# Kernel optimization log

Measured on AMD Instinct MI355X. Metric: run time of the kernel, lower is better.

Reference implementation:

```python
import jax, jax.numpy as jnp
import numpy as np

B, Q, V, T = 96, 96, 197, 77   # image batch, text batch, visual tokens, text tokens
DV, DT, E = 768, 768, 512      # visual_size, textual_size, embed_size


def l2norm(x):
    # F.normalize(t, dim=-1, p=2) with eps=1e-12
    n = jnp.linalg.norm(x, axis=-1, keepdims=True)
    return x / jnp.maximum(n, 1e-12)


def setup_inputs() -> dict:
    key = jax.random.key(0)
    ks = jax.random.split(key, 12)
    sv = 1.0 / np.sqrt(DV).astype(np.float32)
    st = 1.0 / np.sqrt(DT).astype(np.float32)
    return {
        "visual_cls": jax.random.normal(ks[0], (B, DV), jnp.float32),
        "visual_tokens": jax.random.normal(ks[1], (B, V, DV), jnp.float32),
        "textual_cls": jax.random.normal(ks[2], (Q, DT), jnp.float32),
        "textual_tokens": jax.random.normal(ks[3], (Q, T, DT), jnp.float32),
        "Wv_cls": jax.random.normal(ks[4], (E, DV), jnp.float32) * sv,
        "bv_cls": jnp.zeros((E,), jnp.float32),
        "Wt_cls": jax.random.normal(ks[5], (E, DT), jnp.float32) * st,
        "bt_cls": jnp.zeros((E,), jnp.float32),
        "Wv_tok": jax.random.normal(ks[6], (E, DV), jnp.float32) * sv,
        "bv_tok": jnp.zeros((E,), jnp.float32),
        "Wt_tok": jax.random.normal(ks[7], (E, DT), jnp.float32) * st,
        "bt_tok": jnp.zeros((E,), jnp.float32),
        "text_length": jax.random.randint(ks[8], (Q,), 5, T + 1, jnp.int32),
    }


def reference(visual_cls, visual_tokens, textual_cls, textual_tokens,
              Wv_cls, bv_cls, Wt_cls, bt_cls,
              Wv_tok, bv_tok, Wt_tok, bt_tok, text_length):
    # Linear projections (torch nn.Linear: y = x @ W.T + b)
    v_cls = visual_cls @ Wv_cls.T + bv_cls            # [b, e]
    t_cls = textual_cls @ Wt_cls.T + bt_cls           # [q, e]
    v_tok = l2norm(jnp.einsum('bvd,ed->bve', visual_tokens, Wv_tok) + bv_tok)   # [b, v, e]
    t_tok = l2norm(jnp.einsum('qtd,ed->qte', textual_tokens, Wt_tok) + bt_tok)  # [q, t, e]

    # valid-token mask from caption lengths: mask[q, t]
    mask = (jnp.arange(T)[None, :] < text_length[:, None]).astype(v_tok.dtype)

    # fine-grained token similarity: [b, q, v, t], masked on text tokens
    logits = jnp.einsum('bve,qte->bqvt', v_tok, t_tok) * mask[None, :, None, :]

    text_sum = mask.sum(-1)                           # [q]
    t2v = logits.max(axis=2).sum(axis=2) / text_sum[None, :]   # [b, q]
    v2t = logits.max(axis=3).sum(axis=2) / V                   # [b, q]
    return (v_cls, t_cls, t2v, v2t)
```

## Files before the change

kernel.cpp:

```cpp
#include <hip/hip_runtime.h>

#define NB 96
#define NQ 96
#define NV 197
#define NT 77
#define DK 768
#define DE 512

typedef __attribute__((ext_vector_type(8))) short s16x8;
typedef __attribute__((ext_vector_type(4))) float f32x4;

__device__ __forceinline__ unsigned short f2bf(float f) {
  union { float f; unsigned int u; } v; v.f = f;
  unsigned int u = v.u;
  unsigned int r = u + 0x7fffu + ((u >> 16) & 1u);
  return (unsigned short)(r >> 16);
}

__device__ __forceinline__ unsigned int pack2bf(float a, float b) {
  return (unsigned int)f2bf(a) | ((unsigned int)f2bf(b) << 16);
}

#define GL16(gp, lp, off)                                                \
  __builtin_amdgcn_global_load_lds(                                      \
      (const __attribute__((address_space(1))) void*)(gp),               \
      (__attribute__((address_space(3))) void*)(lp), 16, (off), 0)

__global__ __launch_bounds__(256) void cvt_bf16_kernel(
    const float* __restrict__ src, unsigned short* __restrict__ dst, int n4) {
  int i = blockIdx.x * 256 + threadIdx.x;
  if (i < n4) {
    float4 x = ((const float4*)src)[i];
    ushort4 h;
    h.x = f2bf(x.x); h.y = f2bf(x.y); h.z = f2bf(x.z); h.w = f2bf(x.w);
    ((ushort4*)dst)[i] = h;
  }
}

__global__ __launch_bounds__(256) void cls_kernel(
    const float* __restrict__ X, const float* __restrict__ W,
    const float* __restrict__ bias, float* __restrict__ out) {
  __shared__ float xs[DK];
  const int row = blockIdx.x;
  const float* xr = X + (long)row * DK;
  for (int i = threadIdx.x; i < DK; i += 256) xs[i] = xr[i];
  __syncthreads();
  for (int c = threadIdx.x; c < DE; c += 256) {
    const float* wr = W + (long)c * DK;
    float s = 0.f;
    #pragma unroll 4
    for (int k = 0; k < DK; k += 4) {
      float4 w4 = *(const float4*)(wr + k);
      s += xs[k] * w4.x + xs[k + 1] * w4.y + xs[k + 2] * w4.z + xs[k + 3] * w4.w;
    }
    out[(long)row * DE + c] = s + bias[c];
  }
}

__global__ __launch_bounds__(256, 2) void proj_norm_kernel(
    const float* __restrict__ X, const unsigned short* __restrict__ Wb,
    const float* __restrict__ bias, unsigned short* __restrict__ Y, int M) {
  __shared__ __align__(16) unsigned short Ws[512 * 64];
  __shared__ __align__(16) unsigned short Xs[64 * 64];
  __shared__ float ssq_lds[4][64];

  const int tid = threadIdx.x;
  const int wave = tid >> 6;
  const int lane = tid & 63;
  const int l15 = lane & 15;
  const int quad = lane >> 4;
  const long row0 = (long)blockIdx.x * 64;

  const int sub = lane >> 3;
  const int swz = ((lane & 7) ^ sub) << 3;
  const unsigned short* pw_base = Wb + (long)(wave * 8 + sub) * DK + swz;

  const int xrow_a = tid >> 3;
  const int xrow_b = xrow_a + 32;
  const int xs8 = tid & 7;
  long gra = row0 + xrow_a; if (gra > M - 1) gra = M - 1;
  long grb = row0 + xrow_b; if (grb > M - 1) grb = M - 1;
  const float* px_a = X + gra * DK + xs8 * 8;
  const float* px_b = X + grb * DK + xs8 * 8;
  const int xaddr_a = (xrow_a << 6) + ((xs8 ^ (xrow_a & 7)) << 3);
  const int xaddr_b = (xrow_b << 6) + ((xs8 ^ (xrow_b & 7)) << 3);

  f32x4 acc[4][8];
  #pragma unroll
  for (int m = 0; m < 4; ++m)
    #pragma unroll
    for (int n = 0; n < 8; ++n)
      acc[m][n] = (f32x4){0.f, 0.f, 0.f, 0.f};

  for (int kc = 0; kc < DK; kc += 64) {
    __syncthreads();
    {
      float4 x0 = *(const float4*)(px_a);
      float4 x1 = *(const float4*)(px_a + 4);
      uint4 h;
      h.x = pack2bf(x0.x, x0.y); h.y = pack2bf(x0.z, x0.w);
      h.z = pack2bf(x1.x, x1.y); h.w = pack2bf(x1.z, x1.w);
      *(uint4*)(&Xs[xaddr_a]) = h;
      x0 = *(const float4*)(px_b);
      x1 = *(const float4*)(px_b + 4);
      h.x = pack2bf(x0.x, x0.y); h.y = pack2bf(x0.z, x0.w);
      h.z = pack2bf(x1.x, x1.y); h.w = pack2bf(x1.z, x1.w);
      *(uint4*)(&Xs[xaddr_b]) = h;
      px_a += 64; px_b += 64;
    }
    {
      const unsigned short* pw = pw_base;
      #pragma unroll
      for (int j = 0; j < 16; ++j) {
        GL16(pw, &Ws[(j * 4 + wave) << 9], 0);
        pw += 32 * DK;
      }
      pw_base += 64;
    }
    __syncthreads();
    #pragma unroll
    for (int ks = 0; ks < 2; ++ks) {
      s16x8 af[4];
      #pragma unroll
      for (int mi = 0; mi < 4; ++mi) {
        int arow = mi * 16 + l15;
        af[mi] = *(const s16x8*)&Xs[(arow << 6) + ((((ks << 2) + quad) ^ (arow & 7)) << 3)];
      }
      #pragma unroll
      for (int nt = 0; nt < 8; ++nt) {
        int wrow = wave * 128 + nt * 16 + l15;
        s16x8 bfr = *(const s16x8*)&Ws[(wrow << 6) + ((((ks << 2) + quad) ^ (wrow & 7)) << 3)];
        #pragma unroll
        for (int mi = 0; mi < 4; ++mi)
          acc[mi][nt] = __builtin_amdgcn_mfma_f32_16x16x32_bf16(af[mi], bfr, acc[mi][nt], 0, 0, 0);
      }
    }
  }

  #pragma unroll
  for (int nt = 0; nt < 8; ++nt) {
    float bc = bias[wave * 128 + nt * 16 + l15];
    #pragma unroll
    for (int mi = 0; mi < 4; ++mi) {
      acc[mi][nt].x += bc; acc[mi][nt].y += bc; acc[mi][nt].z += bc; acc[mi][nt].w += bc;
    }
  }

  #pragma unroll
  for (int mi = 0; mi < 4; ++mi)
    #pragma unroll
    for (int r = 0; r < 4; ++r) {
      float t = 0.f;
      #pragma unroll
      for (int nt = 0; nt < 8; ++nt) { float v = acc[mi][nt][r]; t += v * v; }
      t += __shfl_xor(t, 1);
      t += __shfl_xor(t, 2);
      t += __shfl_xor(t, 4);
      t += __shfl_xor(t, 8);
      if (l15 == 0) ssq_lds[wave][mi * 16 + quad * 4 + r] = t;
    }
  __syncthreads();

  #pragma unroll
  for (int mi = 0; mi < 4; ++mi) {
    #pragma unroll
    for (int r = 0; r < 4; ++r) {
      int rr = mi * 16 + quad * 4 + r;
      float tot = ssq_lds[0][rr] + ssq_lds[1][rr] + ssq_lds[2][rr] + ssq_lds[3][rr];
      float scale = 1.f / fmaxf(sqrtf(tot), 1e-12f);
      long grow = row0 + rr;
      if (grow < M) {
        #pragma unroll
        for (int nt = 0; nt < 8; ++nt) {
          int col = wave * 128 + nt * 16 + l15;
          Y[grow * DE + col] = f2bf(acc[mi][nt][r] * scale);
        }
      }
    }
  }
}

__global__ __launch_bounds__(256, 2) void score_kernel(
    const unsigned short* __restrict__ Yv, const unsigned short* __restrict__ Yt,
    const int* __restrict__ tlen, float* __restrict__ t2v, float* __restrict__ v2t) {
  __shared__ __align__(16) unsigned short As[208 * 64];
  __shared__ __align__(16) unsigned short Bs[160 * 64];
  __shared__ float colbuf[4][160];
  __shared__ float rowsum_lds[4][2];

  const int tid = threadIdx.x;
  const int wave = tid >> 6;
  const int lane = tid & 63;
  const int l15 = lane & 15;
  const int quad = lane >> 4;

  const int idx = blockIdx.x;
  const int span = idx / 384;
  const int r0 = idx - span * 384;
  const int b = span * 8 + (r0 & 7);
  const int qi = r0 >> 3;
  const int q0 = qi * 2;

  const unsigned short* Ab = Yv + (long)b * (NV * DE);
  const unsigned short* Bb = Yt + (long)q0 * (NT * DE);

  const int sub = lane >> 3;
  const int swz = ((lane & 7) ^ sub) << 3;
  const unsigned short* pA[7];
  #pragma unroll
  for (int j = 0; j < 6; ++j) {
    int row = (j * 4 + wave) * 8 + sub;
    pA[j] = Ab + row * DE + swz;
  }
  {
    int row = (24 + (wave & 1)) * 8 + sub;
    if (row > NV - 1) row = NV - 1;
    pA[6] = Ab + row * DE + swz;
  }
  const unsigned short* pB[5];
  #pragma unroll
  for (int j = 0; j < 5; ++j) {
    int r = (j * 4 + wave) * 8 + sub;
    int half = (r >= 80) ? 1 : 0;
    int t = r - 80 * half;
    if (t > NT - 1) t = NT - 1;
    pB[j] = Bb + (long)half * (NT * DE) + t * DE + swz;
  }

  int aoff[4][2], boff[10][2];
  #pragma unroll
  for (int i = 0; i < 4; ++i) {
    int arow = (wave + i * 4) * 16 + l15;
    #pragma unroll
    for (int ks = 0; ks < 2; ++ks)
      aoff[i][ks] = (arow << 6) + ((((ks << 2) + quad) ^ (arow & 7)) << 3);
  }
  #pragma unroll
  for (int nt = 0; nt < 10; ++nt) {
    int brow = nt * 16 + l15;
    #pragma unroll
    for (int ks = 0; ks < 2; ++ks)
      boff[nt][ks] = (brow << 6) + ((((ks << 2) + quad) ^ (brow & 7)) << 3);
  }

  f32x4 acc[4][10];
  #pragma unroll
  for (int i = 0; i < 4; ++i)
    #pragma unroll
    for (int nt = 0; nt < 10; ++nt)
      acc[i][nt] = (f32x4){0.f, 0.f, 0.f, 0.f};

  auto do_compute = [&]() {
    #pragma unroll
    for (int ks = 0; ks < 2; ++ks) {
      s16x8 bf[10];
      #pragma unroll
      for (int nt = 0; nt < 10; ++nt)
        bf[nt] = *(const s16x8*)&Bs[boff[nt][ks]];
      #pragma unroll
      for (int i = 0; i < 4; ++i) {
        int mt = wave + (i << 2);
        if (mt < 13) {
          s16x8 af = *(const s16x8*)&As[aoff[i][ks]];
          #pragma unroll
          for (int nt = 0; nt < 10; ++nt)
            acc[i][nt] = __builtin_amdgcn_mfma_f32_16x16x32_bf16(af, bf[nt], acc[i][nt], 0, 0, 0);
        }
      }
    }
  };

#define SCORE_STAGE(KB)                                                  \
  {                                                                      \
    _Pragma("unroll")                                                    \
    for (int j = 0; j < 6; ++j)                                          \
      GL16(pA[j], &As[(j * 4 + wave) << 9], KB);                         \
    if (wave >= 2)                                                       \
      GL16(pA[6], &As[(24 + (wave & 1)) << 9], KB);                      \
    _Pragma("unroll")                                                    \
    for (int j = 0; j < 5; ++j)                                          \
      GL16(pB[j], &Bs[(j * 4 + wave) << 9], KB);                         \
  }

#define SCORE_ITER(KB) { __syncthreads(); SCORE_STAGE(KB); __syncthreads(); do_compute(); }

  SCORE_ITER(0)
  SCORE_ITER(128)
  SCORE_ITER(256)
  SCORE_ITER(384)
  SCORE_ITER(512)
  SCORE_ITER(640)
  SCORE_ITER(768)
  SCORE_ITER(896)

#undef SCORE_ITER
#undef SCORE_STAGE

  const int len0 = tlen[q0];
  const int len1 = tlen[q0 + 1];

  #pragma unroll
  for (int nt = 0; nt < 10; ++nt) {
    float m = -1e30f;
    #pragma unroll
    for (int i = 0; i < 4; ++i) {
      int mt = wave + (i << 2);
      if (mt < 13) {
        int mbase = mt * 16 + quad * 4;
        #pragma unroll
        for (int r = 0; r < 4; ++r)
          if (mbase + r < NV) m = fmaxf(m, acc[i][nt][r]);
      }
    }
    m = fmaxf(m, __shfl_xor(m, 16));
    m = fmaxf(m, __shfl_xor(m, 32));
    if (lane < 16) colbuf[wave][nt * 16 + l15] = m;
  }

  float psum[2] = {0.f, 0.f};
  #pragma unroll
  for (int h = 0; h < 2; ++h) {
    int len = h ? len1 : len0;
    #pragma unroll
    for (int i = 0; i < 4; ++i) {
      int mt = wave + (i << 2);
      if (mt < 13) {
        int mbase = mt * 16 + quad * 4;
        #pragma unroll
        for (int r = 0; r < 4; ++r) {
          float rm = -1e30f;
          #pragma unroll
          for (int nt = 0; nt < 5; ++nt) {
            int c = nt * 16 + l15;
            if (c < len) rm = fmaxf(rm, acc[i][h * 5 + nt][r]);
          }
          rm = fmaxf(rm, __shfl_xor(rm, 1));
          rm = fmaxf(rm, __shfl_xor(rm, 2));
          rm = fmaxf(rm, __shfl_xor(rm, 4));
          rm = fmaxf(rm, __shfl_xor(rm, 8));
          if (len < NT) rm = fmaxf(rm, 0.f);
          if (l15 == 0 && (mbase + r) < NV) psum[h] += rm;
        }
      }
    }
    psum[h] += __shfl_xor(psum[h], 16);
    psum[h] += __shfl_xor(psum[h], 32);
  }
  if (lane == 0) { rowsum_lds[wave][0] = psum[0]; rowsum_lds[wave][1] = psum[1]; }
  __syncthreads();

  if (wave < 2) {
    int q = q0 + wave;
    int len = wave ? len1 : len0;
    int cbase = wave * 80;
    float ssum = 0.f;
    for (int c = lane; c < 80; c += 64) {
      if (c < len) {
        float m = fmaxf(fmaxf(colbuf[0][cbase + c], colbuf[1][cbase + c]),
                        fmaxf(colbuf[2][cbase + c], colbuf[3][cbase + c]));
        ssum += m;
      }
    }
    ssum += __shfl_xor(ssum, 1);
    ssum += __shfl_xor(ssum, 2);
    ssum += __shfl_xor(ssum, 4);
    ssum += __shfl_xor(ssum, 8);
    ssum += __shfl_xor(ssum, 16);
    ssum += __shfl_xor(ssum, 32);
    if (lane == 0) {
      float rs = rowsum_lds[0][wave] + rowsum_lds[1][wave] +
                 rowsum_lds[2][wave] + rowsum_lds[3][wave];
      t2v[b * NQ + q] = ssum / (float)len;
      v2t[b * NQ + q] = rs / (float)NV;
    }
  }
}

extern "C" void kernel_launch(void* const* d_in, const int* in_sizes, int n_in,
                              void* d_out, int out_size, void* d_ws, size_t ws_size,
                              hipStream_t stream) {
  (void)in_sizes; (void)n_in; (void)out_size; (void)ws_size;
  const float* visual_cls     = (const float*)d_in[0];
  const float* visual_tokens  = (const float*)d_in[1];
  const float* textual_cls    = (const float*)d_in[2];
  const float* textual_tokens = (const float*)d_in[3];
  const float* Wv_cls = (const float*)d_in[4];
  const float* bv_cls = (const float*)d_in[5];
  const float* Wt_cls = (const float*)d_in[6];
  const float* bt_cls = (const float*)d_in[7];
  const float* Wv_tok = (const float*)d_in[8];
  const float* bv_tok = (const float*)d_in[9];
  const float* Wt_tok = (const float*)d_in[10];
  const float* bt_tok = (const float*)d_in[11];
  const int* text_length = (const int*)d_in[12];

  float* out = (float*)d_out;
  float* v_cls_o = out;
  float* t_cls_o = out + 49152;
  float* t2v_o   = out + 98304;
  float* v2t_o   = out + 107520;

  char* ws = (char*)d_ws;
  unsigned short* Wvb = (unsigned short*)(ws);
  unsigned short* Wtb = (unsigned short*)(ws + 786432);
  unsigned short* Yv  = (unsigned short*)(ws + 1572864);
  unsigned short* Yt  = (unsigned short*)(ws + 20938752);

  cvt_bf16_kernel<<<384, 256, 0, stream>>>(Wv_tok, Wvb, 98304);
  cvt_bf16_kernel<<<384, 256, 0, stream>>>(Wt_tok, Wtb, 98304);

  cls_kernel<<<NB, 256, 0, stream>>>(visual_cls, Wv_cls, bv_cls, v_cls_o);
  cls_kernel<<<NQ, 256, 0, stream>>>(textual_cls, Wt_cls, bt_cls, t_cls_o);

  proj_norm_kernel<<<296, 256, 0, stream>>>(visual_tokens, Wvb, bv_tok, Yv, NB * NV);
  proj_norm_kernel<<<116, 256, 0, stream>>>(textual_tokens, Wtb, bt_tok, Yt, NQ * NT);

  score_kernel<<<(NB * NQ) / 2, 256, 0, stream>>>(Yv, Yt, text_length, t2v_o, v2t_o);
}
```

Measured before the change: 494.0 us.

## Double-buffer score kernel LDS tiles and merge prep/projection launches

The score kernel now uses two LDS buffers with K-chunks of 32 instead of one buffer with chunks of 64. The next chunk's global-to-LDS load is issued before computing on the current one, which halves the barriers per step and overlaps load latency with MFMA work. The weight conversions and CLS projections are fused into one prep kernel, and the two projection-normalize launches become a single grid, removing launch gaps and tail underutilization. Risks are twice as many iterations with smaller MFMA batches per sync, and a new swizzled LDS layout that must stay bank-conflict-free.

```diff
diff --git a/kernel.cpp b/kernel.cpp
--- a/kernel.cpp
+++ b/kernel.cpp
@@ -26,26 +26,38 @@
       (const __attribute__((address_space(1))) void*)(gp),               \
       (__attribute__((address_space(3))) void*)(lp), 16, (off), 0)
 
-__global__ __launch_bounds__(256) void cvt_bf16_kernel(
-    const float* __restrict__ src, unsigned short* __restrict__ dst, int n4) {
-  int i = blockIdx.x * 256 + threadIdx.x;
-  if (i < n4) {
+__global__ __launch_bounds__(256) void prep_kernel(
+    const float* __restrict__ Wv_tok, unsigned short* __restrict__ Wvb,
+    const float* __restrict__ Wt_tok, unsigned short* __restrict__ Wtb,
+    const float* __restrict__ visual_cls, const float* __restrict__ Wv_cls,
+    const float* __restrict__ bv_cls, float* __restrict__ v_cls_o,
+    const float* __restrict__ textual_cls, const float* __restrict__ Wt_cls,
+    const float* __restrict__ bt_cls, float* __restrict__ t_cls_o) {
+  __shared__ float xs[DK];
+  const int blk = blockIdx.x;
+  const int tid = threadIdx.x;
+
+  if (blk < 768) {
+    const float* src = (blk < 384) ? Wv_tok : Wt_tok;
+    unsigned short* dst = (blk < 384) ? Wvb : Wtb;
+    int i = ((blk < 384) ? blk : (blk - 384)) * 256 + tid;
     float4 x = ((const float4*)src)[i];
     ushort4 h;
     h.x = f2bf(x.x); h.y = f2bf(x.y); h.z = f2bf(x.z); h.w = f2bf(x.w);
     ((ushort4*)dst)[i] = h;
-  }
-}
-
-__global__ __launch_bounds__(256) void cls_kernel(
-    const float* __restrict__ X, const float* __restrict__ W,
-    const float* __restrict__ bias, float* __restrict__ out) {
-  __shared__ float xs[DK];
-  const int row = blockIdx.x;
+    return;
+  }
+  const int is_t = (blk >= 864);
+  const int row = blk - (is_t ? 864 : 768);
+  const float* X = is_t ? textual_cls : visual_cls;
+  const float* W = is_t ? Wt_cls : Wv_cls;
+  const float* bias = is_t ? bt_cls : bv_cls;
+  float* out = is_t ? t_cls_o : v_cls_o;
+
   const float* xr = X + (long)row * DK;
-  for (int i = threadIdx.x; i < DK; i += 256) xs[i] = xr[i];
+  for (int i = tid; i < DK; i += 256) xs[i] = xr[i];
   __syncthreads();
-  for (int c = threadIdx.x; c < DE; c += 256) {
+  for (int c = tid; c < DE; c += 256) {
     const float* wr = W + (long)c * DK;
     float s = 0.f;
     #pragma unroll 4
@@ -58,18 +70,28 @@
 }
 
 __global__ __launch_bounds__(256, 2) void proj_norm_kernel(
-    const float* __restrict__ X, const unsigned short* __restrict__ Wb,
-    const float* __restrict__ bias, unsigned short* __restrict__ Y, int M) {
+    const float* __restrict__ Xv, const unsigned short* __restrict__ Wvb,
+    const float* __restrict__ bv, unsigned short* __restrict__ Yv,
+    const float* __restrict__ Xt, const unsigned short* __restrict__ Wtb,
+    const float* __restrict__ bt, unsigned short* __restrict__ Yt) {
   __shared__ __align__(16) unsigned short Ws[512 * 64];
   __shared__ __align__(16) unsigned short Xs[64 * 64];
   __shared__ float ssq_lds[4][64];
+
+  const int blk = blockIdx.x;
+  const int is_t = (blk >= 296);
+  const float* X = is_t ? Xt : Xv;
+  const unsigned short* Wb = is_t ? Wtb : Wvb;
+  const float* bias = is_t ? bt : bv;
+  unsigned short* Y = is_t ? Yt : Yv;
+  const int M = is_t ? (NQ * NT) : (NB * NV);
+  const long row0 = (long)(is_t ? (blk - 296) : blk) * 64;
 
   const int tid = threadIdx.x;
   const int wave = tid >> 6;
   const int lane = tid & 63;
   const int l15 = lane & 15;
   const int quad = lane >> 4;
-  const long row0 = (long)blockIdx.x * 64;
 
   const int sub = lane >> 3;
   const int swz = ((lane & 7) ^ sub) << 3;
@@ -183,8 +205,8 @@
 __global__ __launch_bounds__(256, 2) void score_kernel(
     const unsigned short* __restrict__ Yv, const unsigned short* __restrict__ Yt,
     const int* __restrict__ tlen, float* __restrict__ t2v, float* __restrict__ v2t) {
-  __shared__ __align__(16) unsigned short As[208 * 64];
-  __shared__ __align__(16) unsigned short Bs[160 * 64];
+  __shared__ __align__(16) unsigned short As[2][104 * 64];
+  __shared__ __align__(16) unsigned short Bs[2][80 * 64];
   __shared__ float colbuf[4][160];
   __shared__ float rowsum_lds[4][2];
 
@@ -204,43 +226,40 @@
   const unsigned short* Ab = Yv + (long)b * (NV * DE);
   const unsigned short* Bb = Yt + (long)q0 * (NT * DE);
 
-  const int sub = lane >> 3;
-  const int swz = ((lane & 7) ^ sub) << 3;
-  const unsigned short* pA[7];
-  #pragma unroll
-  for (int j = 0; j < 6; ++j) {
-    int row = (j * 4 + wave) * 8 + sub;
-    pA[j] = Ab + row * DE + swz;
-  }
-  {
-    int row = (24 + (wave & 1)) * 8 + sub;
+  const int ul = lane >> 3;
+  const int slot = lane & 7;
+  const int kseg = ((slot >> 1) ^ (ul & 3)) << 3;
+  const unsigned short* pA[4];
+  #pragma unroll
+  for (int j = 0; j < 4; ++j) {
+    int s = wave + j * 4;
+    int row = (s * 8 + ul) * 2 + (slot & 1);
     if (row > NV - 1) row = NV - 1;
-    pA[6] = Ab + row * DE + swz;
-  }
-  const unsigned short* pB[5];
-  #pragma unroll
-  for (int j = 0; j < 5; ++j) {
-    int r = (j * 4 + wave) * 8 + sub;
+    pA[j] = Ab + row * DE + kseg;
+  }
+  const unsigned short* pB[3];
+  #pragma unroll
+  for (int j = 0; j < 3; ++j) {
+    int s = (j < 2) ? (wave + j * 4) : (wave + 8);
+    int r = (s * 8 + ul) * 2 + (slot & 1);
     int half = (r >= 80) ? 1 : 0;
     int t = r - 80 * half;
     if (t > NT - 1) t = NT - 1;
-    pB[j] = Bb + (long)half * (NT * DE) + t * DE + swz;
-  }
-
-  int aoff[4][2], boff[10][2];
+    pB[j] = Bb + (long)half * (NT * DE) + t * DE + kseg;
+  }
+
+  int aoff[4], boff[10];
   #pragma unroll
   for (int i = 0; i < 4; ++i) {
     int arow = (wave + i * 4) * 16 + l15;
-    #pragma unroll
-    for (int ks = 0; ks < 2; ++ks)
-      aoff[i][ks] = (arow << 6) + ((((ks << 2) + quad) ^ (arow & 7)) << 3);
+    int u = arow >> 1;
+    aoff[i] = (u << 6) + (((quad ^ (u & 3)) << 4)) + ((arow & 1) << 3);
   }
   #pragma unroll
   for (int nt = 0; nt < 10; ++nt) {
     int brow = nt * 16 + l15;
-    #pragma unroll
-    for (int ks = 0; ks < 2; ++ks)
-      boff[nt][ks] = (brow << 6) + ((((ks << 2) + quad) ^ (brow & 7)) << 3);
+    int u = brow >> 1;
+    boff[nt] = (u << 6) + (((quad ^ (u & 3)) << 4)) + ((brow & 1) << 3);
   }
 
   f32x4 acc[4][10];
@@ -250,48 +269,61 @@
     for (int nt = 0; nt < 10; ++nt)
       acc[i][nt] = (f32x4){0.f, 0.f, 0.f, 0.f};
 
-  auto do_compute = [&]() {
-    #pragma unroll
-    for (int ks = 0; ks < 2; ++ks) {
-      s16x8 bf[10];
-      #pragma unroll
-      for (int nt = 0; nt < 10; ++nt)
-        bf[nt] = *(const s16x8*)&Bs[boff[nt][ks]];
-      #pragma unroll
-      for (int i = 0; i < 4; ++i) {
-        int mt = wave + (i << 2);
-        if (mt < 13) {
-          s16x8 af = *(const s16x8*)&As[aoff[i][ks]];
-          #pragma unroll
-          for (int nt = 0; nt < 10; ++nt)
-            acc[i][nt] = __builtin_amdgcn_mfma_f32_16x16x32_bf16(af, bf[nt], acc[i][nt], 0, 0, 0);
-        }
+  auto do_compute = [&](int p) {
+    s16x8 bf[10];
+    #pragma unroll
+    for (int nt = 0; nt < 10; ++nt)
+      bf[nt] = *(const s16x8*)&Bs[p][boff[nt]];
+    #pragma unroll
+    for (int i = 0; i < 4; ++i) {
+      int mt = wave + (i << 2);
+      if (mt < 13) {
+        s16x8 af = *(const s16x8*)&As[p][aoff[i]];
+        #pragma unroll
+        for (int nt = 0; nt < 10; ++nt)
+          acc[i][nt] = __builtin_amdgcn_mfma_f32_16x16x32_bf16(af, bf[nt], acc[i][nt], 0, 0, 0);
       }
     }
   };
 
-#define SCORE_STAGE(KB)                                                  \
+#define SCORE_STAGE(p, KB)                                               \
   {                                                                      \
     _Pragma("unroll")                                                    \
-    for (int j = 0; j < 6; ++j)                                          \
-      GL16(pA[j], &As[(j * 4 + wave) << 9], KB);                         \
-    if (wave >= 2)                                                       \
-      GL16(pA[6], &As[(24 + (wave & 1)) << 9], KB);                      \
+    for (int j = 0; j < 3; ++j)                                          \
+      GL16(pA[j], &As[p][(wave + j * 4) << 9], KB);                      \
+    if (wave == 0)                                                       \
+      GL16(pA[3], &As[p][12 << 9], KB);                                  \
     _Pragma("unroll")                                                    \
-    for (int j = 0; j < 5; ++j)                                          \
-      GL16(pB[j], &Bs[(j * 4 + wave) << 9], KB);                         \
-  }
-
-#define SCORE_ITER(KB) { __syncthreads(); SCORE_STAGE(KB); __syncthreads(); do_compute(); }
-
-  SCORE_ITER(0)
-  SCORE_ITER(128)
-  SCORE_ITER(256)
-  SCORE_ITER(384)
-  SCORE_ITER(512)
-  SCORE_ITER(640)
-  SCORE_ITER(768)
-  SCORE_ITER(896)
+    for (int j = 0; j < 2; ++j)                                          \
+      GL16(pB[j], &Bs[p][(wave + j * 4) << 9], KB);                      \
+    if (wave < 2)                                                        \
+      GL16(pB[2], &Bs[p][(wave + 8) << 9], KB);                          \
+  }
+
+#define SCORE_ITER(cur, KB_NEXT)                                         \
+  {                                                                      \
+    __syncthreads();                                                     \
+    if ((KB_NEXT) < 1024) SCORE_STAGE(1 - (cur), KB_NEXT);               \
+    do_compute(cur);                                                     \
+  }
+
+  SCORE_STAGE(0, 0)
+  SCORE_ITER(0, 64)
+  SCORE_ITER(1, 128)
+  SCORE_ITER(0, 192)
+  SCORE_ITER(1, 256)
+  SCORE_ITER(0, 320)
+  SCORE_ITER(1, 384)
+  SCORE_ITER(0, 448)
+  SCORE_ITER(1, 512)
+  SCORE_ITER(0, 576)
+  SCORE_ITER(1, 640)
+  SCORE_ITER(0, 704)
+  SCORE_ITER(1, 768)
+  SCORE_ITER(0, 832)
+  SCORE_ITER(1, 896)
+  SCORE_ITER(0, 960)
+  SCORE_ITER(1, 1024)
 
 #undef SCORE_ITER
 #undef SCORE_STAGE
@@ -406,14 +438,14 @@
   unsigned short* Yv  = (unsigned short*)(ws + 1572864);
   unsigned short* Yt  = (unsigned short*)(ws + 20938752);
 
-  cvt_bf16_kernel<<<384, 256, 0, stream>>>(Wv_tok, Wvb, 98304);
-  cvt_bf16_kernel<<<384, 256, 0, stream>>>(Wt_tok, Wtb, 98304);
-
-  cls_kernel<<<NB, 256, 0, stream>>>(visual_cls, Wv_cls, bv_cls, v_cls_o);
-  cls_kernel<<<NQ, 256, 0, stream>>>(textual_cls, Wt_cls, bt_cls, t_cls_o);
-
-  proj_norm_kernel<<<296, 256, 0, stream>>>(visual_tokens, Wvb, bv_tok, Yv, NB * NV);
-  proj_norm_kernel<<<116, 256, 0, stream>>>(textual_tokens, Wtb, bt_tok, Yt, NQ * NT);
+  prep_kernel<<<960, 256, 0, stream>>>(
+      Wv_tok, Wvb, Wt_tok, Wtb,
+      visual_cls, Wv_cls, bv_cls, v_cls_o,
+      textual_cls, Wt_cls, bt_cls, t_cls_o);
+
+  proj_norm_kernel<<<412, 256, 0, stream>>>(
+      visual_tokens, Wvb, bv_tok, Yv,
+      textual_tokens, Wtb, bt_tok, Yt);
 
   score_kernel<<<(NB * NQ) / 2, 256, 0, stream>>>(Yv, Yt, text_length, t2v_o, v2t_o);
 }
```

New measurement: 439.5 us. 1.12x faster.
